# Kernel tuning notes

Measured on AMD Instinct MI355X. Metric: run time of the kernel, lower is better.

Reference implementation:

```python
import jax, jax.numpy as jnp
import numpy as np

B, S, H, NH = 4, 1024, 768, 12
HD = H // NH  # 64
ALPHA = 32.0


def setup_inputs() -> dict:
    key = jax.random.key(0)
    ks = jax.random.split(key, 8)
    scale = 0.02
    return {
        "hidden_states": jax.random.normal(ks[0], (B, S, H), jnp.float32),
        "attention_mask": jnp.zeros((B, 1, 1, S), jnp.float32),
        "rel_pos": jax.random.normal(ks[1], (B, NH, S, S), jnp.float32),
        "rel_2d_pos": jax.random.normal(ks[2], (B, NH, S, S), jnp.float32),
        "Wq": jax.random.normal(ks[3], (H, H), jnp.float32) * scale,
        "bq": jnp.zeros((H,), jnp.float32),
        "Wk": jax.random.normal(ks[4], (H, H), jnp.float32) * scale,
        "bk": jnp.zeros((H,), jnp.float32),
        "Wv": jax.random.normal(ks[5], (H, H), jnp.float32) * scale,
        "bv": jnp.zeros((H,), jnp.float32),
    }


def _split_heads(x):
    # [B, S, H] -> [B, NH, S, HD]
    return x.reshape(B, S, NH, HD).transpose(0, 2, 1, 3)


def _cogview_softmax(scores, alpha=ALPHA):
    # PB-Relax: divide by alpha, subtract row max, re-scale by alpha, softmax.
    scaled = scores / alpha
    m = jnp.max(scaled, axis=-1, keepdims=True)
    return jax.nn.softmax((scaled - m) * alpha, axis=-1)


def reference(hidden_states, attention_mask, rel_pos, rel_2d_pos, Wq, bq, Wk, bk, Wv, bv):
    norm = jnp.sqrt(jnp.float32(HD))
    q = _split_heads(hidden_states @ Wq + bq)  # [B,NH,S,HD]
    k = _split_heads(hidden_states @ Wk + bk)
    v = _split_heads(hidden_states @ Wv + bv)
    scores = jnp.einsum("bhqd,bhkd->bhqk", q / norm, k)  # [B,NH,S,S]
    scores = scores + (rel_pos + rel_2d_pos) / norm
    scores = scores + attention_mask  # broadcast [B,1,1,S]
    probs = _cogview_softmax(scores)
    ctx = jnp.einsum("bhqk,bhkd->bhqd", probs, v)  # [B,NH,S,HD]
    return ctx.transpose(0, 2, 1, 3).reshape(B, S, H)
```

## Files before the change

### kernel.cpp

```cpp
#include <hip/hip_runtime.h>
#include <hip/hip_bf16.h>

#define BB 4
#define SS 1024
#define HH 768
#define NHH 12
#define HDD 64

typedef __attribute__((ext_vector_type(8))) short s8v;
typedef __attribute__((ext_vector_type(4))) float f4v;
typedef __attribute__((ext_vector_type(4))) unsigned int u4v;
typedef __attribute__((ext_vector_type(2))) unsigned int u2v;

__device__ __forceinline__ unsigned int pkbf(float a, float b){
    union { __hip_bfloat162 h; unsigned int u; } c;
    c.h = __float22bfloat162_rn(make_float2(a, b));
    return c.u;
}

__global__ __launch_bounds__(256) void k_convert_x(const float* __restrict__ x,
                                                   unsigned short* __restrict__ xb){
    int i = (blockIdx.x * 256 + threadIdx.x) * 8;
    f4v a = *(const f4v*)(x + i);
    f4v b = *(const f4v*)(x + i + 4);
    u4v o = { pkbf(a[0],a[1]), pkbf(a[2],a[3]), pkbf(b[0],b[1]), pkbf(b[2],b[3]) };
    *(u4v*)(xb + i) = o;
}

__global__ __launch_bounds__(256) void k_transpose_w(const float* __restrict__ Wq,
                                                     const float* __restrict__ Wk,
                                                     const float* __restrict__ Wv,
                                                     unsigned short* __restrict__ Wt){
    __shared__ float tile[32][33];
    const int w = blockIdx.z;
    const float* W = (w == 0) ? Wq : ((w == 1) ? Wk : Wv);
    const int tx = threadIdx.x & 31, ty = threadIdx.x >> 5;
    const int c0 = blockIdx.x * 32, r0 = blockIdx.y * 32;
    #pragma unroll
    for (int j = 0; j < 4; ++j)
        tile[ty + 8*j][tx] = W[(size_t)(r0 + ty + 8*j) * HH + c0 + tx];
    __syncthreads();
    unsigned short* Wo = Wt + (size_t)w * HH * HH;
    #pragma unroll
    for (int j = 0; j < 4; ++j){
        float v = tile[tx][ty + 8*j];
        Wo[(size_t)(c0 + ty + 8*j) * HH + r0 + tx] = (unsigned short)(pkbf(v, 0.f) & 0xffffu);
    }
}

__global__ __launch_bounds__(256, 2) void k_gemm_qkv(const unsigned short* __restrict__ Xb,
                                                     const unsigned short* __restrict__ Wt,
                                                     const float* __restrict__ bq,
                                                     const float* __restrict__ bk,
                                                     const float* __restrict__ bv,
                                                     unsigned short* __restrict__ Qb,
                                                     unsigned short* __restrict__ Kb,
                                                     unsigned short* __restrict__ Vt){
    const int w  = blockIdx.z;
    const int m0 = blockIdx.x * 128, n0 = blockIdx.y * 128;
    const int l  = threadIdx.x & 63, wid = threadIdx.x >> 6;
    const int wm = wid >> 1, wn = wid & 1;
    const int lc = l & 15,  lg = l >> 4;
    const unsigned short* Wb = Wt + (size_t)w * HH * HH;

    f4v acc[4][4];
    #pragma unroll
    for (int i = 0; i < 4; ++i)
        #pragma unroll
        for (int j = 0; j < 4; ++j) acc[i][j] = (f4v)0.f;

    const int arow = m0 + wm * 64 + lc;
    const int brow = n0 + wn * 64 + lc;
    for (int k0 = 0; k0 < HH; k0 += 32){
        s8v af[4], bfr[4];
        #pragma unroll
        for (int mt = 0; mt < 4; ++mt)
            af[mt] = *(const s8v*)(Xb + (size_t)(arow + mt*16) * HH + k0 + lg*8);
        #pragma unroll
        for (int nt = 0; nt < 4; ++nt)
            bfr[nt] = *(const s8v*)(Wb + (size_t)(brow + nt*16) * HH + k0 + lg*8);
        #pragma unroll
        for (int mt = 0; mt < 4; ++mt)
            #pragma unroll
            for (int nt = 0; nt < 4; ++nt)
                acc[mt][nt] = __builtin_amdgcn_mfma_f32_16x16x32_bf16(af[mt], bfr[nt], acc[mt][nt], 0, 0, 0);
    }

    const float* bias = (w == 0) ? bq : ((w == 1) ? bk : bv);
    const float scale = (w == 0) ? 0.125f : 1.0f;
    float bv4[4];
    #pragma unroll
    for (int nt = 0; nt < 4; ++nt) bv4[nt] = bias[n0 + wn*64 + nt*16 + lc];

    if (w < 2){
        unsigned short* dst = (w == 0) ? Qb : Kb;
        #pragma unroll
        for (int mt = 0; mt < 4; ++mt){
            #pragma unroll
            for (int nt = 0; nt < 4; ++nt){
                const int nn = n0 + wn*64 + nt*16 + lc;
                const int hh = nn >> 6, dd = nn & 63;
                #pragma unroll
                for (int r = 0; r < 4; ++r){
                    const int mm = m0 + wm*64 + mt*16 + lg*4 + r;
                    const int bb = mm >> 10, ss = mm & 1023;
                    const float v = (acc[mt][nt][r] + bv4[nt]) * scale;
                    dst[(((size_t)bb*NHH + hh)*SS + ss)*HDD + dd] = (unsigned short)(pkbf(v, 0.f) & 0xffffu);
                }
            }
        }
    } else {
        #pragma unroll
        for (int mt = 0; mt < 4; ++mt){
            const int sbase = m0 + wm*64 + mt*16 + lg*4;
            const int bb = sbase >> 10, ss = sbase & 1023;
            #pragma unroll
            for (int nt = 0; nt < 4; ++nt){
                const int nn = n0 + wn*64 + nt*16 + lc;
                const int hh = nn >> 6, dd = nn & 63;
                u2v pk2 = { pkbf(acc[mt][nt][0] + bv4[nt], acc[mt][nt][1] + bv4[nt]),
                            pkbf(acc[mt][nt][2] + bv4[nt], acc[mt][nt][3] + bv4[nt]) };
                *(u2v*)(Vt + (((size_t)bb*NHH + hh)*HDD + dd)*SS + ss) = pk2;
            }
        }
    }
}

__global__ __launch_bounds__(256, 6) void k_attn(const unsigned short* __restrict__ Qb,
                                                 const unsigned short* __restrict__ Kb,
                                                 const unsigned short* __restrict__ Vt,
                                                 const float* __restrict__ rel1,
                                                 const float* __restrict__ rel2,
                                                 const float* __restrict__ mask,
                                                 float* __restrict__ out){
    __shared__ float red[4][64][17];
    const int l  = threadIdx.x & 63, wid = threadIdx.x >> 6;
    const int lc = l & 15, lg = l >> 4;
    const int qblk = blockIdx.x, h = blockIdx.y, b = blockIdx.z;
    const int bh = b * NHH + h;
    const int q0 = qblk * 16;
    const int q  = q0 + lc;

    const unsigned short* Qrow = Qb + ((size_t)bh * SS + q) * HDD;
    const s8v qf0 = *(const s8v*)(Qrow + lg * 8);
    const s8v qf1 = *(const s8v*)(Qrow + 32 + lg * 8);
    const unsigned short* Kbase = Kb + (size_t)bh * SS * HDD;
    const unsigned short* Vbase = Vt + (size_t)bh * HDD * SS;
    const float* r1 = rel1 + ((size_t)bh * SS + q) * SS;
    const float* r2 = rel2 + ((size_t)bh * SS + q) * SS;
    const float* mk = mask + (size_t)b * SS;

    f4v accO[4];
    #pragma unroll
    for (int i = 0; i < 4; ++i) accO[i] = (f4v)0.f;
    float lsum = 0.f;

    const int srcA = (lg & 1) * 32 + lc, srcB = srcA + 16;
    const bool hif = (l >= 32);

    for (int t = 0; t < 4; ++t){
        const int kk0 = (wid * 4 + t) * 64;

        f4v r1v[4], r2v[4], mkv[4];
        #pragma unroll
        for (int mt = 0; mt < 4; ++mt){
            const int col = kk0 + mt*16 + lg*4;
            r1v[mt] = *(const f4v*)(r1 + col);
            r2v[mt] = *(const f4v*)(r2 + col);
            mkv[mt] = *(const f4v*)(mk + col);
        }

        f4v accS[4];
        #pragma unroll
        for (int mt = 0; mt < 4; ++mt) accS[mt] = (f4v)0.f;
        #pragma unroll
        for (int ks = 0; ks < 2; ++ks){
            const s8v qf = ks ? qf1 : qf0;
            #pragma unroll
            for (int mt = 0; mt < 4; ++mt){
                const s8v kf = *(const s8v*)(Kbase + (size_t)(kk0 + mt*16 + lc) * HDD + ks*32 + lg*8);
                accS[mt] = __builtin_amdgcn_mfma_f32_16x16x32_bf16(kf, qf, accS[mt], 0, 0, 0);
            }
        }

        unsigned int v0[4], v1[4];
        #pragma unroll
        for (int mt = 0; mt < 4; ++mt){
            const float p0 = __expf(accS[mt][0] + (r1v[mt][0] + r2v[mt][0]) * 0.125f + mkv[mt][0]);
            const float p1 = __expf(accS[mt][1] + (r1v[mt][1] + r2v[mt][1]) * 0.125f + mkv[mt][1]);
            const float p2 = __expf(accS[mt][2] + (r1v[mt][2] + r2v[mt][2]) * 0.125f + mkv[mt][2]);
            const float p3 = __expf(accS[mt][3] + (r1v[mt][3] + r2v[mt][3]) * 0.125f + mkv[mt][3]);
            lsum += (p0 + p1) + (p2 + p3);
            v0[mt] = pkbf(p0, p1);
            v1[mt] = pkbf(p2, p3);
        }

        #pragma unroll
        for (int ks = 0; ks < 2; ++ks){
            const unsigned int a0 = __shfl(v0[2*ks], srcA), b0 = __shfl(v0[2*ks+1], srcA);
            const unsigned int a1 = __shfl(v1[2*ks], srcA), b1 = __shfl(v1[2*ks+1], srcA);
            const unsigned int a2 = __shfl(v0[2*ks], srcB), b2 = __shfl(v0[2*ks+1], srcB);
            const unsigned int a3 = __shfl(v1[2*ks], srcB), b3 = __shfl(v1[2*ks+1], srcB);
            union { unsigned int u[4]; s8v s; } pu;
            pu.u[0] = hif ? b0 : a0;
            pu.u[1] = hif ? b1 : a1;
            pu.u[2] = hif ? b2 : a2;
            pu.u[3] = hif ? b3 : a3;
            const s8v pf = pu.s;
            #pragma unroll
            for (int nt = 0; nt < 4; ++nt){
                const s8v vf = *(const s8v*)(Vbase + (size_t)(nt*16 + lc) * SS + kk0 + ks*32 + lg*8);
                accO[nt] = __builtin_amdgcn_mfma_f32_16x16x32_bf16(pf, vf, accO[nt], 0, 0, 0);
            }
        }
    }

    lsum += __shfl_xor(lsum, 16);
    lsum += __shfl_xor(lsum, 32);

    #pragma unroll
    for (int nt = 0; nt < 4; ++nt)
        #pragma unroll
        for (int r = 0; r < 4; ++r)
            red[wid][l][nt*4 + r] = accO[nt][r];
    red[wid][l][16] = lsum;
    __syncthreads();

    if (wid == 0){
        #pragma unroll
        for (int w = 1; w < 4; ++w){
            #pragma unroll
            for (int nt = 0; nt < 4; ++nt)
                #pragma unroll
                for (int r = 0; r < 4; ++r)
                    accO[nt][r] += red[w][l][nt*4 + r];
            lsum += red[w][l][16];
        }
        #pragma unroll
        for (int r = 0; r < 4; ++r){
            const float lr  = __shfl(lsum, lg*4 + r);
            const float inv = 1.f / lr;
            const int row = q0 + lg*4 + r;
            float* orow = out + ((size_t)b * SS + row) * HH + h * HDD;
            #pragma unroll
            for (int nt = 0; nt < 4; ++nt)
                orow[nt*16 + lc] = accO[nt][r] * inv;
        }
    }
}

extern "C" void kernel_launch(void* const* d_in, const int* in_sizes, int n_in,
                              void* d_out, int out_size, void* d_ws, size_t ws_size,
                              hipStream_t stream){
    (void)in_sizes; (void)n_in; (void)out_size; (void)ws_size;
    const float* hs   = (const float*)d_in[0];
    const float* mask = (const float*)d_in[1];
    const float* rel1 = (const float*)d_in[2];
    const float* rel2 = (const float*)d_in[3];
    const float* Wq   = (const float*)d_in[4];
    const float* bq   = (const float*)d_in[5];
    const float* Wk   = (const float*)d_in[6];
    const float* bk   = (const float*)d_in[7];
    const float* Wv   = (const float*)d_in[8];
    const float* bv   = (const float*)d_in[9];
    float* out = (float*)d_out;

    unsigned short* Xb = (unsigned short*)d_ws;
    unsigned short* Wt = Xb + 3145728;
    unsigned short* Qb = Wt + 3*589824;
    unsigned short* Kb = Qb + 3145728;
    unsigned short* Vt = Kb + 3145728;

    k_convert_x  <<<1536, 256, 0, stream>>>(hs, Xb);
    k_transpose_w<<<dim3(24, 24, 3), 256, 0, stream>>>(Wq, Wk, Wv, Wt);
    k_gemm_qkv   <<<dim3(32, 6, 3), 256, 0, stream>>>(Xb, Wt, bq, bk, bv, Qb, Kb, Vt);
    k_attn       <<<dim3(64, 12, 4), 256, 0, stream>>>(Qb, Kb, Vt, rel1, rel2, mask, out);
}
```

Measured before the change: 567.9 us.

## Stage combined rel-pos bias through swizzled LDS with coalesced row loads

```diff
diff --git a/kernel.cpp b/kernel.cpp
--- a/kernel.cpp
+++ b/kernel.cpp
@@ -126,28 +126,29 @@
     }
 }
 
-__global__ __launch_bounds__(256, 6) void k_attn(const unsigned short* __restrict__ Qb,
+__global__ __launch_bounds__(256, 8) void k_attn(const unsigned short* __restrict__ Qb,
                                                  const unsigned short* __restrict__ Kb,
                                                  const unsigned short* __restrict__ Vt,
                                                  const float* __restrict__ rel1,
                                                  const float* __restrict__ rel2,
                                                  const float* __restrict__ mask,
                                                  float* __restrict__ out){
-    __shared__ float red[4][64][17];
+    __shared__ float stg[16 * 256];
+    float (*red)[64][17] = (float (*)[64][17])stg;
+
     const int l  = threadIdx.x & 63, wid = threadIdx.x >> 6;
     const int lc = l & 15, lg = l >> 4;
     const int qblk = blockIdx.x, h = blockIdx.y, b = blockIdx.z;
     const int bh = b * NHH + h;
     const int q0 = qblk * 16;
-    const int q  = q0 + lc;
-
-    const unsigned short* Qrow = Qb + ((size_t)bh * SS + q) * HDD;
+
+    const unsigned short* Qrow = Qb + ((size_t)bh * SS + q0 + lc) * HDD;
     const s8v qf0 = *(const s8v*)(Qrow + lg * 8);
     const s8v qf1 = *(const s8v*)(Qrow + 32 + lg * 8);
     const unsigned short* Kbase = Kb + (size_t)bh * SS * HDD;
     const unsigned short* Vbase = Vt + (size_t)bh * HDD * SS;
-    const float* r1 = rel1 + ((size_t)bh * SS + q) * SS;
-    const float* r2 = rel2 + ((size_t)bh * SS + q) * SS;
+    const float* r1 = rel1 + ((size_t)bh * SS + q0) * SS;
+    const float* r2 = rel2 + ((size_t)bh * SS + q0) * SS;
     const float* mk = mask + (size_t)b * SS;
 
     f4v accO[4];
@@ -158,16 +159,28 @@
     const int srcA = (lg & 1) * 32 + lc, srcB = srcA + 16;
     const bool hif = (l >= 32);
 
-    for (int t = 0; t < 4; ++t){
-        const int kk0 = (wid * 4 + t) * 64;
-
-        f4v r1v[4], r2v[4], mkv[4];
-        #pragma unroll
-        for (int mt = 0; mt < 4; ++mt){
-            const int col = kk0 + mt*16 + lg*4;
-            r1v[mt] = *(const f4v*)(r1 + col);
-            r2v[mt] = *(const f4v*)(r2 + col);
-            mkv[mt] = *(const f4v*)(mk + col);
+    for (int st = 0; st < 4; ++st){
+        {
+            const int cb = st * 256 + l * 4;
+            const f4v mv = *(const f4v*)(mk + cb);
+            #pragma unroll
+            for (int j = 0; j < 4; ++j){
+                const int r = wid * 4 + j;
+                const f4v va = *(const f4v*)(r1 + (size_t)r * SS + cb);
+                const f4v vb = *(const f4v*)(r2 + (size_t)r * SS + cb);
+                const f4v sres = (va + vb) * 0.125f + mv;
+                *(f4v*)(stg + r * 256 + ((l * 4) ^ ((r & 7) << 2))) = sres;
+            }
+        }
+        __syncthreads();
+
+        const int kk0 = st * 256 + wid * 64;
+
+        f4v sv[4];
+        #pragma unroll
+        for (int mt = 0; mt < 4; ++mt){
+            const int c = wid * 64 + mt * 16 + lg * 4;
+            sv[mt] = *(const f4v*)(stg + lc * 256 + (c ^ ((lc & 7) << 2)));
         }
 
         f4v accS[4];
@@ -186,10 +199,10 @@
         unsigned int v0[4], v1[4];
         #pragma unroll
         for (int mt = 0; mt < 4; ++mt){
-            const float p0 = __expf(accS[mt][0] + (r1v[mt][0] + r2v[mt][0]) * 0.125f + mkv[mt][0]);
-            const float p1 = __expf(accS[mt][1] + (r1v[mt][1] + r2v[mt][1]) * 0.125f + mkv[mt][1]);
-            const float p2 = __expf(accS[mt][2] + (r1v[mt][2] + r2v[mt][2]) * 0.125f + mkv[mt][2]);
-            const float p3 = __expf(accS[mt][3] + (r1v[mt][3] + r2v[mt][3]) * 0.125f + mkv[mt][3]);
+            const float p0 = __expf(accS[mt][0] + sv[mt][0]);
+            const float p1 = __expf(accS[mt][1] + sv[mt][1]);
+            const float p2 = __expf(accS[mt][2] + sv[mt][2]);
+            const float p3 = __expf(accS[mt][3] + sv[mt][3]);
             lsum += (p0 + p1) + (p2 + p3);
             v0[mt] = pkbf(p0, p1);
             v1[mt] = pkbf(p2, p3);
@@ -213,22 +226,25 @@
                 accO[nt] = __builtin_amdgcn_mfma_f32_16x16x32_bf16(pf, vf, accO[nt], 0, 0, 0);
             }
         }
+        __syncthreads();
     }
 
     lsum += __shfl_xor(lsum, 16);
     lsum += __shfl_xor(lsum, 32);
 
-    #pragma unroll
-    for (int nt = 0; nt < 4; ++nt)
-        #pragma unroll
-        for (int r = 0; r < 4; ++r)
-            red[wid][l][nt*4 + r] = accO[nt][r];
-    red[wid][l][16] = lsum;
+    if (wid){
+        #pragma unroll
+        for (int nt = 0; nt < 4; ++nt)
+            #pragma unroll
+            for (int r = 0; r < 4; ++r)
+                red[wid-1][l][nt*4 + r] = accO[nt][r];
+        red[wid-1][l][16] = lsum;
+    }
     __syncthreads();
 
     if (wid == 0){
         #pragma unroll
-        for (int w = 1; w < 4; ++w){
+        for (int w = 0; w < 3; ++w){
             #pragma unroll
             for (int nt = 0; nt < 4; ++nt)
                 #pragma unroll
```

Result: slower. 609.7 us (+7.4%).
